# Performance work log

Measured on AMD Instinct MI355X. Metric: run time of the kernel, lower is better.

The kernel has to match this reference:

```python
import jax, jax.numpy as jnp
import numpy as np

D = 2048        # hidden_size
F = 1024        # moe_intermediate_size
E = 16          # num_experts
TOP_K = 2       # num_experts_per_tok
NORM_TOPK = True
B, S = 2, 1024


def setup_inputs() -> dict:
    key = jax.random.key(0)
    ks = jax.random.split(key, 6)
    scale = 0.02
    x = jax.random.normal(ks[0], (B, S, D), jnp.float32)
    w_gate = jax.random.normal(ks[1], (D, E), jnp.float32) * scale          # gate Linear (no bias)
    w_g = jax.random.normal(ks[2], (E, D, F), jnp.float32) * scale          # SwitchGLU gate_proj
    w_u = jax.random.normal(ks[3], (E, D, F), jnp.float32) * scale          # SwitchGLU up_proj
    w_d = jax.random.normal(ks[4], (E, F, D), jnp.float32) * scale          # SwitchGLU down_proj
    expert_bias = jnp.zeros((E,), jnp.float32)                              # nn.Parameter(zeros)
    return {"x": x, "w_gate": w_gate, "w_g": w_g, "w_u": w_u, "w_d": w_d,
            "expert_bias": expert_bias}


def reference(x, w_gate, w_g, w_u, w_d, expert_bias):
    xf = x.reshape(-1, D)  # [T, D] flatten tokens
    T = xf.shape[0]
    # routing: softmax in fp32, bias added AFTER softmax (as in source)
    gates = jax.nn.softmax((xf @ w_gate).astype(jnp.float32), axis=-1) + expert_bias
    scores, inds = jax.lax.top_k(gates, TOP_K)  # values gathered from biased gates
    if NORM_TOPK:
        scores = scores / (jnp.sum(scores, axis=-1, keepdims=True) + 1e-20)
    scores = scores.astype(x.dtype)
    # scatter top-k weights into dense [T, E] combine matrix (top-k inds are distinct)
    cw = jnp.zeros((T, E), x.dtype).at[jnp.arange(T)[:, None], inds].add(scores)
    # scan over experts: each step one gated-SiLU MLP + weighted accumulate
    def step(acc, inp):
        wg, wu, wd, w = inp  # wg/wu [D,F], wd [F,D], w [T]
        h = jax.nn.silu(xf @ wg) * (xf @ wu)  # [T, F]
        return acc + w[:, None] * (h @ wd), None
    y, _ = jax.lax.scan(step, jnp.zeros_like(xf), (w_g, w_u, w_d, cw.T))
    return y.reshape(x.shape)
```

## Files before the change

### kernel.cpp

```cpp
#include <hip/hip_runtime.h>
#include <hip/hip_bf16.h>

#define D_DIM 2048
#define F_DIM 1024
#define E_NUM 16
#define T_TOK 2048

typedef float f32x4 __attribute__((ext_vector_type(4)));
typedef short short8 __attribute__((ext_vector_type(8)));

__device__ inline unsigned pk2bf(float a, float b) {
    __hip_bfloat162 h2 = __float22bfloat162_rn(make_float2(a, b));
    union { __hip_bfloat162 h; unsigned u; } c; c.h = h2; return c.u;
}

__global__ __launch_bounds__(64) void k_route(const float* __restrict__ x,
                                              const float* __restrict__ wg,
                                              const float* __restrict__ bias,
                                              int* __restrict__ topk_idx,
                                              float* __restrict__ topk_w,
                                              int* __restrict__ counts) {
    int t = blockIdx.x;
    int l = threadIdx.x;
    int e = l & 15, c = l >> 4;
    const float* xr = x + (size_t)t * D_DIM + c * (D_DIM / 4);
    const float* wr = wg + (size_t)(c * (D_DIM / 4)) * E_NUM + e;
    float acc = 0.f;
#pragma unroll 4
    for (int d = 0; d < D_DIM / 4; ++d) acc += xr[d] * wr[(size_t)d * E_NUM];
    acc += __shfl_xor(acc, 16);
    acc += __shfl_xor(acc, 32);
    float m = acc;
#pragma unroll
    for (int s = 1; s < 16; s <<= 1) m = fmaxf(m, __shfl_xor(m, s));
    float p = __expf(acc - m);
    float sum = p;
#pragma unroll
    for (int s = 1; s < 16; s <<= 1) sum += __shfl_xor(sum, s);
    p = p / sum + bias[e];
    float v1 = p; int i1 = e;
#pragma unroll
    for (int s = 1; s < 16; s <<= 1) {
        float ov = __shfl_xor(v1, s); int oi = __shfl_xor(i1, s);
        if (ov > v1 || (ov == v1 && oi < i1)) { v1 = ov; i1 = oi; }
    }
    float v2 = (e == i1) ? -1e30f : p; int i2 = e;
#pragma unroll
    for (int s = 1; s < 16; s <<= 1) {
        float ov = __shfl_xor(v2, s); int oi = __shfl_xor(i2, s);
        if (ov > v2 || (ov == v2 && oi < i2)) { v2 = ov; i2 = oi; }
    }
    if (l == 0) {
        float s2 = v1 + v2 + 1e-20f;
        topk_idx[2 * t] = i1; topk_idx[2 * t + 1] = i2;
        topk_w[2 * t] = v1 / s2; topk_w[2 * t + 1] = v2 / s2;
        atomicAdd(&counts[i1], 1);
        atomicAdd(&counts[i2], 1);
    }
}

__global__ void k_offsets(const int* __restrict__ counts, int* __restrict__ offsets,
                          int* __restrict__ cursors) {
    if (threadIdx.x == 0) {
        int run = 0;
        for (int e = 0; e < E_NUM; ++e) { offsets[e] = run; cursors[e] = run; run += counts[e]; }
        offsets[E_NUM] = run;
    }
}

__global__ void k_scatter(const int* __restrict__ topk_idx, const float* __restrict__ topk_w,
                          int* __restrict__ cursors, int* __restrict__ token_ids,
                          float* __restrict__ slot_w) {
    int i = blockIdx.x * blockDim.x + threadIdx.x;
    if (i >= T_TOK * 2) return;
    int e = topk_idx[i];
    int slot = atomicAdd(&cursors[e], 1);
    token_ids[slot] = i >> 1;
    slot_w[slot] = topk_w[i];
}

__global__ __launch_bounds__(256, 3) void k_gateup(const float* __restrict__ x,
                                                   const float* __restrict__ wg_all,
                                                   const float* __restrict__ wu_all,
                                                   const int* __restrict__ offsets,
                                                   const int* __restrict__ token_ids,
                                                   __hip_bfloat16* __restrict__ hbuf) {
    int e = blockIdx.z;
    int off = offsets[e];
    int n_e = offsets[e + 1] - off;
    int m0 = blockIdx.y * 128;
    if (m0 >= n_e) return;
    int n0 = blockIdx.x * 64;
    const float* wg = wg_all + (size_t)e * (D_DIM * F_DIM);
    const float* wu = wu_all + (size_t)e * (D_DIM * F_DIM);

    __shared__ unsigned short As[2][128 * 40];
    __shared__ unsigned short Bs[2][2][64 * 40];

    int tid = threadIdx.x;
    int wid = tid >> 6, lane = tid & 63;
    int q = lane >> 4, nl = lane & 15;
    int wr = wid >> 1, wc = wid & 1;

    int arow = tid >> 1, acg = (tid & 1) * 16;
    int ag = m0 + arow;
    bool avalid = ag < n_e;
    const float* xrow = x + (size_t)(avalid ? token_ids[off + ag] : 0) * D_DIM;
    int bkr = (tid >> 4) * 2;
    int bcol = (tid & 15) * 4;

    f32x4 ra[4], rg[2], ru[2];
    f32x4 accG[4][2], accU[4][2];
#pragma unroll
    for (int ms = 0; ms < 4; ++ms)
#pragma unroll
        for (int ns = 0; ns < 2; ++ns) {
            accG[ms][ns] = (f32x4){0.f, 0.f, 0.f, 0.f};
            accU[ms][ns] = (f32x4){0.f, 0.f, 0.f, 0.f};
        }

    auto loadG = [&](int k0) {
#pragma unroll
        for (int j = 0; j < 4; ++j)
            ra[j] = avalid ? *(const f32x4*)(xrow + k0 + acg + 4 * j) : (f32x4){0.f, 0.f, 0.f, 0.f};
        size_t o0 = (size_t)(k0 + bkr) * F_DIM + n0 + bcol;
        rg[0] = *(const f32x4*)(wg + o0);
        rg[1] = *(const f32x4*)(wg + o0 + F_DIM);
        ru[0] = *(const f32x4*)(wu + o0);
        ru[1] = *(const f32x4*)(wu + o0 + F_DIM);
    };
    auto writeL = [&](int b) {
        unsigned short* a = &As[b][arow * 40 + acg];
        union { short8 v; unsigned u[4]; } w0, w1;
        w0.u[0] = pk2bf(ra[0].x, ra[0].y); w0.u[1] = pk2bf(ra[0].z, ra[0].w);
        w0.u[2] = pk2bf(ra[1].x, ra[1].y); w0.u[3] = pk2bf(ra[1].z, ra[1].w);
        w1.u[0] = pk2bf(ra[2].x, ra[2].y); w1.u[1] = pk2bf(ra[2].z, ra[2].w);
        w1.u[2] = pk2bf(ra[3].x, ra[3].y); w1.u[3] = pk2bf(ra[3].z, ra[3].w);
        *(short8*)a = w0.v; *(short8*)(a + 8) = w1.v;
#pragma unroll
        for (int j = 0; j < 4; ++j) {
            int col = bcol + j;
            int kk = bkr ^ (((col >> 3) & 3) << 3);
            *(unsigned*)&Bs[b][0][col * 40 + kk] = pk2bf(rg[0][j], rg[1][j]);
            *(unsigned*)&Bs[b][1][col * 40 + kk] = pk2bf(ru[0][j], ru[1][j]);
        }
    };
    auto compute = [&](int b) {
        short8 af[4];
#pragma unroll
        for (int ms = 0; ms < 4; ++ms)
            af[ms] = *(const short8*)&As[b][(wr * 64 + ms * 16 + nl) * 40 + q * 8];
#pragma unroll
        for (int ns = 0; ns < 2; ++ns) {
            int col = wc * 32 + ns * 16 + nl;
            int colb = col * 40 + 8 * (q ^ ((col >> 3) & 3));
            short8 bg = *(const short8*)&Bs[b][0][colb];
            short8 bu = *(const short8*)&Bs[b][1][colb];
#pragma unroll
            for (int ms = 0; ms < 4; ++ms) {
                accG[ms][ns] = __builtin_amdgcn_mfma_f32_16x16x32_bf16(af[ms], bg, accG[ms][ns], 0, 0, 0);
                accU[ms][ns] = __builtin_amdgcn_mfma_f32_16x16x32_bf16(af[ms], bu, accU[ms][ns], 0, 0, 0);
            }
        }
    };

    loadG(0);
    writeL(0);
    __syncthreads();
    for (int t = 0; t < D_DIM / 32; ++t) {
        int b = t & 1;
        if (t < D_DIM / 32 - 1) loadG((t + 1) * 32);
        compute(b);
        if (t < D_DIM / 32 - 1) writeL(b ^ 1);
        __syncthreads();
    }

#pragma unroll
    for (int ms = 0; ms < 4; ++ms)
#pragma unroll
        for (int j = 0; j < 4; ++j) {
            int g2 = m0 + wr * 64 + ms * 16 + q * 4 + j;
            if (g2 < n_e) {
                size_t hbase = (size_t)(off + g2) * F_DIM;
#pragma unroll
                for (int ns = 0; ns < 2; ++ns) {
                    float g = accG[ms][ns][j];
                    float u = accU[ms][ns][j];
                    float hv = (g / (1.f + __expf(-g))) * u;
                    hbuf[hbase + n0 + wc * 32 + ns * 16 + nl] = __float2bfloat16(hv);
                }
            }
        }
}

__global__ __launch_bounds__(256, 3) void k_down(const __hip_bfloat16* __restrict__ hbuf,
                                                 const float* __restrict__ wd_all,
                                                 const int* __restrict__ offsets,
                                                 const int* __restrict__ token_ids,
                                                 const float* __restrict__ slot_w,
                                                 float* __restrict__ y) {
    int e = blockIdx.z;
    int off = offsets[e];
    int n_e = offsets[e + 1] - off;
    int m0 = blockIdx.y * 128;
    if (m0 >= n_e) return;
    int n0 = blockIdx.x * 64;
    const float* wd = wd_all + (size_t)e * (F_DIM * D_DIM);

    __shared__ unsigned short As[2][128 * 40];
    __shared__ unsigned short Bs[2][64 * 40];

    int tid = threadIdx.x;
    int wid = tid >> 6, lane = tid & 63;
    int q = lane >> 4, nl = lane & 15;
    int wr = wid >> 1, wc = wid & 1;

    int arow = tid >> 1, acg = (tid & 1) * 16;
    int ag = m0 + arow;
    bool avalid = ag < n_e;
    const unsigned short* hrow = (const unsigned short*)hbuf + (size_t)(off + (avalid ? ag : 0)) * F_DIM;
    int bkr = (tid >> 4) * 2;
    int bcol = (tid & 15) * 4;

    short8 rh[2];
    f32x4 rd[2];
    f32x4 acc[4][2];
#pragma unroll
    for (int ms = 0; ms < 4; ++ms)
#pragma unroll
        for (int ns = 0; ns < 2; ++ns) acc[ms][ns] = (f32x4){0.f, 0.f, 0.f, 0.f};

    auto loadG = [&](int k0) {
        if (avalid) {
            rh[0] = *(const short8*)(hrow + k0 + acg);
            rh[1] = *(const short8*)(hrow + k0 + acg + 8);
        } else {
            rh[0] = (short8){0, 0, 0, 0, 0, 0, 0, 0};
            rh[1] = (short8){0, 0, 0, 0, 0, 0, 0, 0};
        }
        size_t o0 = (size_t)(k0 + bkr) * D_DIM + n0 + bcol;
        rd[0] = *(const f32x4*)(wd + o0);
        rd[1] = *(const f32x4*)(wd + o0 + D_DIM);
    };
    auto writeL = [&](int b) {
        unsigned short* a = &As[b][arow * 40 + acg];
        *(short8*)a = rh[0]; *(short8*)(a + 8) = rh[1];
#pragma unroll
        for (int j = 0; j < 4; ++j) {
            int col = bcol + j;
            int kk = bkr ^ (((col >> 3) & 3) << 3);
            *(unsigned*)&Bs[b][col * 40 + kk] = pk2bf(rd[0][j], rd[1][j]);
        }
    };
    auto compute = [&](int b) {
        short8 af[4];
#pragma unroll
        for (int ms = 0; ms < 4; ++ms)
            af[ms] = *(const short8*)&As[b][(wr * 64 + ms * 16 + nl) * 40 + q * 8];
#pragma unroll
        for (int ns = 0; ns < 2; ++ns) {
            int col = wc * 32 + ns * 16 + nl;
            short8 bd = *(const short8*)&Bs[b][col * 40 + 8 * (q ^ ((col >> 3) & 3))];
#pragma unroll
            for (int ms = 0; ms < 4; ++ms)
                acc[ms][ns] = __builtin_amdgcn_mfma_f32_16x16x32_bf16(af[ms], bd, acc[ms][ns], 0, 0, 0);
        }
    };

    loadG(0);
    writeL(0);
    __syncthreads();
    for (int t = 0; t < F_DIM / 32; ++t) {
        int b = t & 1;
        if (t < F_DIM / 32 - 1) loadG((t + 1) * 32);
        compute(b);
        if (t < F_DIM / 32 - 1) writeL(b ^ 1);
        __syncthreads();
    }

#pragma unroll
    for (int ms = 0; ms < 4; ++ms)
#pragma unroll
        for (int j = 0; j < 4; ++j) {
            int g2 = m0 + wr * 64 + ms * 16 + q * 4 + j;
            if (g2 < n_e) {
                float w2 = slot_w[off + g2];
                int t = token_ids[off + g2];
#pragma unroll
                for (int ns = 0; ns < 2; ++ns)
                    atomicAdd(&y[(size_t)t * D_DIM + n0 + wc * 32 + ns * 16 + nl], acc[ms][ns][j] * w2);
            }
        }
}

extern "C" void kernel_launch(void* const* d_in, const int* in_sizes, int n_in,
                              void* d_out, int out_size, void* d_ws, size_t ws_size,
                              hipStream_t stream) {
    const float* x      = (const float*)d_in[0];
    const float* w_gate = (const float*)d_in[1];
    const float* w_g    = (const float*)d_in[2];
    const float* w_u    = (const float*)d_in[3];
    const float* w_d    = (const float*)d_in[4];
    const float* bias   = (const float*)d_in[5];
    float* y = (float*)d_out;

    char* ws = (char*)d_ws;
    int*   counts    = (int*)(ws + 0);
    int*   offsets   = (int*)(ws + 64);
    int*   cursors   = (int*)(ws + 192);
    int*   topk_idx  = (int*)(ws + 256);
    float* topk_w    = (float*)(ws + 256 + 16384);
    int*   token_ids = (int*)(ws + 256 + 32768);
    float* slot_w    = (float*)(ws + 256 + 49152);
    __hip_bfloat16* hbuf = (__hip_bfloat16*)(ws + 66048);

    hipMemsetAsync(ws, 0, 256, stream);
    hipMemsetAsync(d_out, 0, (size_t)out_size * sizeof(float), stream);

    k_route<<<T_TOK, 64, 0, stream>>>(x, w_gate, bias, topk_idx, topk_w, counts);
    k_offsets<<<1, 64, 0, stream>>>(counts, offsets, cursors);
    k_scatter<<<(T_TOK * 2 + 255) / 256, 256, 0, stream>>>(topk_idx, topk_w, cursors, token_ids, slot_w);
    k_gateup<<<dim3(F_DIM / 64, 16, E_NUM), 256, 0, stream>>>(x, w_g, w_u, offsets, token_ids, hbuf);
    k_down<<<dim3(D_DIM / 64, 16, E_NUM), 256, 0, stream>>>(hbuf, w_d, offsets, token_ids, slot_w, y);
}
```

Measured before the change: 329.8 us.

## Deepen global prefetch to two stages with explicit waitcnt and sched barriers

```diff
diff --git a/kernel.cpp b/kernel.cpp
--- a/kernel.cpp
+++ b/kernel.cpp
@@ -8,6 +8,13 @@
 
 typedef float f32x4 __attribute__((ext_vector_type(4)));
 typedef short short8 __attribute__((ext_vector_type(8)));
+
+#define VM8 asm volatile("s_waitcnt vmcnt(8)" ::: "memory")
+#define VM4 asm volatile("s_waitcnt vmcnt(4)" ::: "memory")
+#define VM0 asm volatile("s_waitcnt vmcnt(0)" ::: "memory")
+#define LGKM0 asm volatile("s_waitcnt lgkmcnt(0)" ::: "memory")
+#define SB0 __builtin_amdgcn_sched_barrier(0)
+#define SBAR __builtin_amdgcn_s_barrier()
 
 __device__ inline unsigned pk2bf(float a, float b) {
     __hip_bfloat162 h2 = __float22bfloat162_rn(make_float2(a, b));
@@ -79,7 +86,7 @@
     slot_w[slot] = topk_w[i];
 }
 
-__global__ __launch_bounds__(256, 3) void k_gateup(const float* __restrict__ x,
+__global__ __launch_bounds__(256, 2) void k_gateup(const float* __restrict__ x,
                                                    const float* __restrict__ wg_all,
                                                    const float* __restrict__ wu_all,
                                                    const int* __restrict__ offsets,
@@ -105,11 +112,12 @@
     int arow = tid >> 1, acg = (tid & 1) * 16;
     int ag = m0 + arow;
     bool avalid = ag < n_e;
-    const float* xrow = x + (size_t)(avalid ? token_ids[off + ag] : 0) * D_DIM;
+    const float* xrow = x + (size_t)token_ids[off + (avalid ? ag : 0)] * D_DIM;
     int bkr = (tid >> 4) * 2;
     int bcol = (tid & 15) * 4;
 
-    f32x4 ra[4], rg[2], ru[2];
+    f32x4 raA[4], rgA[2], ruA[2];
+    f32x4 raB[4], rgB[2], ruB[2];
     f32x4 accG[4][2], accU[4][2];
 #pragma unroll
     for (int ms = 0; ms < 4; ++ms)
@@ -119,30 +127,54 @@
             accU[ms][ns] = (f32x4){0.f, 0.f, 0.f, 0.f};
         }
 
-    auto loadG = [&](int k0) {
-#pragma unroll
-        for (int j = 0; j < 4; ++j)
-            ra[j] = avalid ? *(const f32x4*)(xrow + k0 + acg + 4 * j) : (f32x4){0.f, 0.f, 0.f, 0.f};
+    auto loadGA = [&](int k0) {
+#pragma unroll
+        for (int j = 0; j < 4; ++j) raA[j] = *(const f32x4*)(xrow + k0 + acg + 4 * j);
         size_t o0 = (size_t)(k0 + bkr) * F_DIM + n0 + bcol;
-        rg[0] = *(const f32x4*)(wg + o0);
-        rg[1] = *(const f32x4*)(wg + o0 + F_DIM);
-        ru[0] = *(const f32x4*)(wu + o0);
-        ru[1] = *(const f32x4*)(wu + o0 + F_DIM);
-    };
-    auto writeL = [&](int b) {
-        unsigned short* a = &As[b][arow * 40 + acg];
+        rgA[0] = *(const f32x4*)(wg + o0);
+        rgA[1] = *(const f32x4*)(wg + o0 + F_DIM);
+        ruA[0] = *(const f32x4*)(wu + o0);
+        ruA[1] = *(const f32x4*)(wu + o0 + F_DIM);
+    };
+    auto loadGB = [&](int k0) {
+#pragma unroll
+        for (int j = 0; j < 4; ++j) raB[j] = *(const f32x4*)(xrow + k0 + acg + 4 * j);
+        size_t o0 = (size_t)(k0 + bkr) * F_DIM + n0 + bcol;
+        rgB[0] = *(const f32x4*)(wg + o0);
+        rgB[1] = *(const f32x4*)(wg + o0 + F_DIM);
+        ruB[0] = *(const f32x4*)(wu + o0);
+        ruB[1] = *(const f32x4*)(wu + o0 + F_DIM);
+    };
+    auto writeLA = [&]() {
+        unsigned short* a = &As[0][arow * 40 + acg];
         union { short8 v; unsigned u[4]; } w0, w1;
-        w0.u[0] = pk2bf(ra[0].x, ra[0].y); w0.u[1] = pk2bf(ra[0].z, ra[0].w);
-        w0.u[2] = pk2bf(ra[1].x, ra[1].y); w0.u[3] = pk2bf(ra[1].z, ra[1].w);
-        w1.u[0] = pk2bf(ra[2].x, ra[2].y); w1.u[1] = pk2bf(ra[2].z, ra[2].w);
-        w1.u[2] = pk2bf(ra[3].x, ra[3].y); w1.u[3] = pk2bf(ra[3].z, ra[3].w);
+        w0.u[0] = pk2bf(raA[0].x, raA[0].y); w0.u[1] = pk2bf(raA[0].z, raA[0].w);
+        w0.u[2] = pk2bf(raA[1].x, raA[1].y); w0.u[3] = pk2bf(raA[1].z, raA[1].w);
+        w1.u[0] = pk2bf(raA[2].x, raA[2].y); w1.u[1] = pk2bf(raA[2].z, raA[2].w);
+        w1.u[2] = pk2bf(raA[3].x, raA[3].y); w1.u[3] = pk2bf(raA[3].z, raA[3].w);
         *(short8*)a = w0.v; *(short8*)(a + 8) = w1.v;
 #pragma unroll
         for (int j = 0; j < 4; ++j) {
             int col = bcol + j;
             int kk = bkr ^ (((col >> 3) & 3) << 3);
-            *(unsigned*)&Bs[b][0][col * 40 + kk] = pk2bf(rg[0][j], rg[1][j]);
-            *(unsigned*)&Bs[b][1][col * 40 + kk] = pk2bf(ru[0][j], ru[1][j]);
+            *(unsigned*)&Bs[0][0][col * 40 + kk] = pk2bf(rgA[0][j], rgA[1][j]);
+            *(unsigned*)&Bs[0][1][col * 40 + kk] = pk2bf(ruA[0][j], ruA[1][j]);
+        }
+    };
+    auto writeLB = [&]() {
+        unsigned short* a = &As[1][arow * 40 + acg];
+        union { short8 v; unsigned u[4]; } w0, w1;
+        w0.u[0] = pk2bf(raB[0].x, raB[0].y); w0.u[1] = pk2bf(raB[0].z, raB[0].w);
+        w0.u[2] = pk2bf(raB[1].x, raB[1].y); w0.u[3] = pk2bf(raB[1].z, raB[1].w);
+        w1.u[0] = pk2bf(raB[2].x, raB[2].y); w1.u[1] = pk2bf(raB[2].z, raB[2].w);
+        w1.u[2] = pk2bf(raB[3].x, raB[3].y); w1.u[3] = pk2bf(raB[3].z, raB[3].w);
+        *(short8*)a = w0.v; *(short8*)(a + 8) = w1.v;
+#pragma unroll
+        for (int j = 0; j < 4; ++j) {
+            int col = bcol + j;
+            int kk = bkr ^ (((col >> 3) & 3) << 3);
+            *(unsigned*)&Bs[1][0][col * 40 + kk] = pk2bf(rgB[0][j], rgB[1][j]);
+            *(unsigned*)&Bs[1][1][col * 40 + kk] = pk2bf(ruB[0][j], ruB[1][j]);
         }
     };
     auto compute = [&](int b) {
@@ -164,15 +196,27 @@
         }
     };
 
-    loadG(0);
-    writeL(0);
-    __syncthreads();
-    for (int t = 0; t < D_DIM / 32; ++t) {
-        int b = t & 1;
-        if (t < D_DIM / 32 - 1) loadG((t + 1) * 32);
-        compute(b);
-        if (t < D_DIM / 32 - 1) writeL(b ^ 1);
-        __syncthreads();
+    const int NT = D_DIM / 32;
+    loadGA(0);
+    loadGB(32);
+    VM8; SB0;
+    writeLA();
+    LGKM0; SB0; SBAR; SB0;
+    for (int t = 0; t < NT; t += 2) {
+        if (t + 2 < NT) loadGA((t + 2) * 32);
+        compute(0);
+        if (t + 2 < NT) { VM8; } else { VM0; }
+        SB0;
+        writeLB();
+        LGKM0; SB0; SBAR; SB0;
+        if (t + 3 < NT) loadGB((t + 3) * 32);
+        compute(1);
+        if (t + 2 < NT) {
+            if (t + 4 < NT) { VM8; } else { VM0; }
+            SB0;
+            writeLA();
+            LGKM0; SB0; SBAR; SB0;
+        }
     }
 
 #pragma unroll
@@ -193,7 +237,7 @@
         }
 }
 
-__global__ __launch_bounds__(256, 3) void k_down(const __hip_bfloat16* __restrict__ hbuf,
+__global__ __launch_bounds__(256, 2) void k_down(const __hip_bfloat16* __restrict__ hbuf,
                                                  const float* __restrict__ wd_all,
                                                  const int* __restrict__ offsets,
                                                  const int* __restrict__ token_ids,
@@ -222,34 +266,46 @@
     int bkr = (tid >> 4) * 2;
     int bcol = (tid & 15) * 4;
 
-    short8 rh[2];
-    f32x4 rd[2];
+    short8 rhA[2], rhB[2];
+    f32x4 rdA[2], rdB[2];
     f32x4 acc[4][2];
 #pragma unroll
     for (int ms = 0; ms < 4; ++ms)
 #pragma unroll
         for (int ns = 0; ns < 2; ++ns) acc[ms][ns] = (f32x4){0.f, 0.f, 0.f, 0.f};
 
-    auto loadG = [&](int k0) {
-        if (avalid) {
-            rh[0] = *(const short8*)(hrow + k0 + acg);
-            rh[1] = *(const short8*)(hrow + k0 + acg + 8);
-        } else {
-            rh[0] = (short8){0, 0, 0, 0, 0, 0, 0, 0};
-            rh[1] = (short8){0, 0, 0, 0, 0, 0, 0, 0};
-        }
+    auto loadGA = [&](int k0) {
+        rhA[0] = *(const short8*)(hrow + k0 + acg);
+        rhA[1] = *(const short8*)(hrow + k0 + acg + 8);
         size_t o0 = (size_t)(k0 + bkr) * D_DIM + n0 + bcol;
-        rd[0] = *(const f32x4*)(wd + o0);
-        rd[1] = *(const f32x4*)(wd + o0 + D_DIM);
-    };
-    auto writeL = [&](int b) {
-        unsigned short* a = &As[b][arow * 40 + acg];
-        *(short8*)a = rh[0]; *(short8*)(a + 8) = rh[1];
+        rdA[0] = *(const f32x4*)(wd + o0);
+        rdA[1] = *(const f32x4*)(wd + o0 + D_DIM);
+    };
+    auto loadGB = [&](int k0) {
+        rhB[0] = *(const short8*)(hrow + k0 + acg);
+        rhB[1] = *(const short8*)(hrow + k0 + acg + 8);
+        size_t o0 = (size_t)(k0 + bkr) * D_DIM + n0 + bcol;
+        rdB[0] = *(const f32x4*)(wd + o0);
+        rdB[1] = *(const f32x4*)(wd + o0 + D_DIM);
+    };
+    auto writeLA = [&]() {
+        unsigned short* a = &As[0][arow * 40 + acg];
+        *(short8*)a = rhA[0]; *(short8*)(a + 8) = rhA[1];
 #pragma unroll
         for (int j = 0; j < 4; ++j) {
             int col = bcol + j;
             int kk = bkr ^ (((col >> 3) & 3) << 3);
-            *(unsigned*)&Bs[b][col * 40 + kk] = pk2bf(rd[0][j], rd[1][j]);
+            *(unsigned*)&Bs[0][col * 40 + kk] = pk2bf(rdA[0][j], rdA[1][j]);
+        }
+    };
+    auto writeLB = [&]() {
+        unsigned short* a = &As[1][arow * 40 + acg];
+        *(short8*)a = rhB[0]; *(short8*)(a + 8) = rhB[1];
+#pragma unroll
+        for (int j = 0; j < 4; ++j) {
+            int col = bcol + j;
+            int kk = bkr ^ (((col >> 3) & 3) << 3);
+            *(unsigned*)&Bs[1][col * 40 + kk] = pk2bf(rdB[0][j], rdB[1][j]);
         }
     };
     auto compute = [&](int b) {
@@ -267,15 +323,27 @@
         }
     };
 
-    loadG(0);
-    writeL(0);
-    __syncthreads();
-    for (int t = 0; t < F_DIM / 32; ++t) {
-        int b = t & 1;
-        if (t < F_DIM / 32 - 1) loadG((t + 1) * 32);
-        compute(b);
-        if (t < F_DIM / 32 - 1) writeL(b ^ 1);
-        __syncthreads();
+    const int NT = F_DIM / 32;
+    loadGA(0);
+    loadGB(32);
+    VM4; SB0;
+    writeLA();
+    LGKM0; SB0; SBAR; SB0;
+    for (int t = 0; t < NT; t += 2) {
+        if (t + 2 < NT) loadGA((t + 2) * 32);
+        compute(0);
+        if (t + 2 < NT) { VM4; } else { VM0; }
+        SB0;
+        writeLB();
+        LGKM0; SB0; SBAR; SB0;
+        if (t + 3 < NT) loadGB((t + 3) * 32);
+        compute(1);
+        if (t + 2 < NT) {
+            if (t + 4 < NT) { VM4; } else { VM0; }
+            SB0;
+            writeLA();
+            LGKM0; SB0; SBAR; SB0;
+        }
     }
 
 #pragma unroll
```

Measured after the change: 360.0 us. +9.2%, slower.

## Pre-gather tokens to bf16 and widen GEMM tiles to 128x128 with 512 threads

Applied to the files above, without the earlier changes.

```diff
diff --git a/kernel.cpp b/kernel.cpp
--- a/kernel.cpp
+++ b/kernel.cpp
@@ -5,9 +5,11 @@
 #define F_DIM 1024
 #define E_NUM 16
 #define T_TOK 2048
+#define NSLOT (T_TOK * 2)
 
 typedef float f32x4 __attribute__((ext_vector_type(4)));
 typedef short short8 __attribute__((ext_vector_type(8)));
+typedef unsigned uint2v __attribute__((ext_vector_type(2)));
 
 __device__ inline unsigned pk2bf(float a, float b) {
     __hip_bfloat162 h2 = __float22bfloat162_rn(make_float2(a, b));
@@ -72,44 +74,60 @@
                           int* __restrict__ cursors, int* __restrict__ token_ids,
                           float* __restrict__ slot_w) {
     int i = blockIdx.x * blockDim.x + threadIdx.x;
-    if (i >= T_TOK * 2) return;
+    if (i >= NSLOT) return;
     int e = topk_idx[i];
     int slot = atomicAdd(&cursors[e], 1);
     token_ids[slot] = i >> 1;
     slot_w[slot] = topk_w[i];
 }
 
-__global__ __launch_bounds__(256, 3) void k_gateup(const float* __restrict__ x,
+__global__ __launch_bounds__(256) void k_gather(const float* __restrict__ x,
+                                                const int* __restrict__ token_ids,
+                                                __hip_bfloat16* __restrict__ xg) {
+    int s = blockIdx.x;
+    const float* src = x + (size_t)token_ids[s] * D_DIM + threadIdx.x * 8;
+    f32x4 a = *(const f32x4*)src;
+    f32x4 b = *(const f32x4*)(src + 4);
+    union { short8 v; unsigned u[4]; } w;
+    w.u[0] = pk2bf(a.x, a.y); w.u[1] = pk2bf(a.z, a.w);
+    w.u[2] = pk2bf(b.x, b.y); w.u[3] = pk2bf(b.z, b.w);
+    *(short8*)((unsigned short*)xg + (size_t)s * D_DIM + threadIdx.x * 8) = w.v;
+}
+
+__global__ __launch_bounds__(512, 2) void k_gateup(const __hip_bfloat16* __restrict__ xg,
                                                    const float* __restrict__ wg_all,
                                                    const float* __restrict__ wu_all,
                                                    const int* __restrict__ offsets,
-                                                   const int* __restrict__ token_ids,
                                                    __hip_bfloat16* __restrict__ hbuf) {
     int e = blockIdx.z;
     int off = offsets[e];
     int n_e = offsets[e + 1] - off;
     int m0 = blockIdx.y * 128;
     if (m0 >= n_e) return;
-    int n0 = blockIdx.x * 64;
+    int n0 = blockIdx.x * 128;
     const float* wg = wg_all + (size_t)e * (D_DIM * F_DIM);
     const float* wu = wu_all + (size_t)e * (D_DIM * F_DIM);
 
     __shared__ unsigned short As[2][128 * 40];
-    __shared__ unsigned short Bs[2][2][64 * 40];
+    __shared__ unsigned short Bs[2][2][128 * 40];
 
     int tid = threadIdx.x;
     int wid = tid >> 6, lane = tid & 63;
     int q = lane >> 4, nl = lane & 15;
-    int wr = wid >> 1, wc = wid & 1;
-
-    int arow = tid >> 1, acg = (tid & 1) * 16;
-    int ag = m0 + arow;
-    bool avalid = ag < n_e;
-    const float* xrow = x + (size_t)(avalid ? token_ids[off + ag] : 0) * D_DIM;
-    int bkr = (tid >> 4) * 2;
-    int bcol = (tid & 15) * 4;
-
-    f32x4 ra[4], rg[2], ru[2];
+    int wm = wid >> 2, wn = wid & 3;
+
+    int arow = tid >> 2, acg = (tid & 3) * 8;
+    int sg = off + m0 + arow; if (sg > NSLOT - 1) sg = NSLOT - 1;
+    const unsigned short* xrow = (const unsigned short*)xg + (size_t)sg * D_DIM;
+
+    int bmat = tid >> 8;
+    int t8 = tid & 255;
+    int bcol = (t8 & 31) * 4;
+    int bk4 = (t8 >> 5) * 4;
+    const float* wmat = bmat ? wu : wg;
+
+    short8 rA;
+    f32x4 rw[4];
     f32x4 accG[4][2], accU[4][2];
 #pragma unroll
     for (int ms = 0; ms < 4; ++ms)
@@ -120,39 +138,31 @@
         }
 
     auto loadG = [&](int k0) {
-#pragma unroll
-        for (int j = 0; j < 4; ++j)
-            ra[j] = avalid ? *(const f32x4*)(xrow + k0 + acg + 4 * j) : (f32x4){0.f, 0.f, 0.f, 0.f};
-        size_t o0 = (size_t)(k0 + bkr) * F_DIM + n0 + bcol;
-        rg[0] = *(const f32x4*)(wg + o0);
-        rg[1] = *(const f32x4*)(wg + o0 + F_DIM);
-        ru[0] = *(const f32x4*)(wu + o0);
-        ru[1] = *(const f32x4*)(wu + o0 + F_DIM);
+        rA = *(const short8*)(xrow + k0 + acg);
+        const float* p = wmat + (size_t)(k0 + bk4) * F_DIM + n0 + bcol;
+#pragma unroll
+        for (int i = 0; i < 4; ++i) rw[i] = *(const f32x4*)(p + (size_t)i * F_DIM);
     };
     auto writeL = [&](int b) {
-        unsigned short* a = &As[b][arow * 40 + acg];
-        union { short8 v; unsigned u[4]; } w0, w1;
-        w0.u[0] = pk2bf(ra[0].x, ra[0].y); w0.u[1] = pk2bf(ra[0].z, ra[0].w);
-        w0.u[2] = pk2bf(ra[1].x, ra[1].y); w0.u[3] = pk2bf(ra[1].z, ra[1].w);
-        w1.u[0] = pk2bf(ra[2].x, ra[2].y); w1.u[1] = pk2bf(ra[2].z, ra[2].w);
-        w1.u[2] = pk2bf(ra[3].x, ra[3].y); w1.u[3] = pk2bf(ra[3].z, ra[3].w);
-        *(short8*)a = w0.v; *(short8*)(a + 8) = w1.v;
+        *(short8*)&As[b][arow * 40 + acg] = rA;
 #pragma unroll
         for (int j = 0; j < 4; ++j) {
             int col = bcol + j;
-            int kk = bkr ^ (((col >> 3) & 3) << 3);
-            *(unsigned*)&Bs[b][0][col * 40 + kk] = pk2bf(rg[0][j], rg[1][j]);
-            *(unsigned*)&Bs[b][1][col * 40 + kk] = pk2bf(ru[0][j], ru[1][j]);
+            int kk = bk4 ^ (((col >> 3) & 3) << 3);
+            uint2v v;
+            v[0] = pk2bf(rw[0][j], rw[1][j]);
+            v[1] = pk2bf(rw[2][j], rw[3][j]);
+            *(uint2v*)&Bs[b][bmat][col * 40 + kk] = v;
         }
     };
     auto compute = [&](int b) {
         short8 af[4];
 #pragma unroll
         for (int ms = 0; ms < 4; ++ms)
-            af[ms] = *(const short8*)&As[b][(wr * 64 + ms * 16 + nl) * 40 + q * 8];
+            af[ms] = *(const short8*)&As[b][(wm * 64 + ms * 16 + nl) * 40 + q * 8];
 #pragma unroll
         for (int ns = 0; ns < 2; ++ns) {
-            int col = wc * 32 + ns * 16 + nl;
+            int col = wn * 32 + ns * 16 + nl;
             int colb = col * 40 + 8 * (q ^ ((col >> 3) & 3));
             short8 bg = *(const short8*)&Bs[b][0][colb];
             short8 bu = *(const short8*)&Bs[b][1][colb];
@@ -179,21 +189,21 @@
     for (int ms = 0; ms < 4; ++ms)
 #pragma unroll
         for (int j = 0; j < 4; ++j) {
-            int g2 = m0 + wr * 64 + ms * 16 + q * 4 + j;
-            if (g2 < n_e) {
-                size_t hbase = (size_t)(off + g2) * F_DIM;
+            int r = m0 + wm * 64 + ms * 16 + q * 4 + j;
+            if (r < n_e) {
+                size_t hbase = (size_t)(off + r) * F_DIM;
 #pragma unroll
                 for (int ns = 0; ns < 2; ++ns) {
                     float g = accG[ms][ns][j];
                     float u = accU[ms][ns][j];
                     float hv = (g / (1.f + __expf(-g))) * u;
-                    hbuf[hbase + n0 + wc * 32 + ns * 16 + nl] = __float2bfloat16(hv);
+                    hbuf[hbase + n0 + wn * 32 + ns * 16 + nl] = __float2bfloat16(hv);
                 }
             }
         }
 }
 
-__global__ __launch_bounds__(256, 3) void k_down(const __hip_bfloat16* __restrict__ hbuf,
+__global__ __launch_bounds__(512, 4) void k_down(const __hip_bfloat16* __restrict__ hbuf,
                                                  const float* __restrict__ wd_all,
                                                  const int* __restrict__ offsets,
                                                  const int* __restrict__ token_ids,
@@ -204,25 +214,25 @@
     int n_e = offsets[e + 1] - off;
     int m0 = blockIdx.y * 128;
     if (m0 >= n_e) return;
-    int n0 = blockIdx.x * 64;
+    int n0 = blockIdx.x * 128;
     const float* wd = wd_all + (size_t)e * (F_DIM * D_DIM);
 
     __shared__ unsigned short As[2][128 * 40];
-    __shared__ unsigned short Bs[2][64 * 40];
+    __shared__ unsigned short Bs[2][128 * 40];
 
     int tid = threadIdx.x;
     int wid = tid >> 6, lane = tid & 63;
     int q = lane >> 4, nl = lane & 15;
-    int wr = wid >> 1, wc = wid & 1;
-
-    int arow = tid >> 1, acg = (tid & 1) * 16;
-    int ag = m0 + arow;
-    bool avalid = ag < n_e;
-    const unsigned short* hrow = (const unsigned short*)hbuf + (size_t)(off + (avalid ? ag : 0)) * F_DIM;
-    int bkr = (tid >> 4) * 2;
-    int bcol = (tid & 15) * 4;
-
-    short8 rh[2];
+    int wm = wid >> 2, wn = wid & 3;
+
+    int arow = tid >> 2, acg = (tid & 3) * 8;
+    int sg = off + m0 + arow; if (sg > NSLOT - 1) sg = NSLOT - 1;
+    const unsigned short* hrow = (const unsigned short*)hbuf + (size_t)sg * F_DIM;
+
+    int bcol = (tid & 31) * 4;
+    int bk2 = (tid >> 5) * 2;
+
+    short8 rA;
     f32x4 rd[2];
     f32x4 acc[4][2];
 #pragma unroll
@@ -231,24 +241,17 @@
         for (int ns = 0; ns < 2; ++ns) acc[ms][ns] = (f32x4){0.f, 0.f, 0.f, 0.f};
 
     auto loadG = [&](int k0) {
-        if (avalid) {
-            rh[0] = *(const short8*)(hrow + k0 + acg);
-            rh[1] = *(const short8*)(hrow + k0 + acg + 8);
-        } else {
-            rh[0] = (short8){0, 0, 0, 0, 0, 0, 0, 0};
-            rh[1] = (short8){0, 0, 0, 0, 0, 0, 0, 0};
-        }
-        size_t o0 = (size_t)(k0 + bkr) * D_DIM + n0 + bcol;
+        rA = *(const short8*)(hrow + k0 + acg);
+        size_t o0 = (size_t)(k0 + bk2) * D_DIM + n0 + bcol;
         rd[0] = *(const f32x4*)(wd + o0);
         rd[1] = *(const f32x4*)(wd + o0 + D_DIM);
     };
     auto writeL = [&](int b) {
-        unsigned short* a = &As[b][arow * 40 + acg];
-        *(short8*)a = rh[0]; *(short8*)(a + 8) = rh[1];
+        *(short8*)&As[b][arow * 40 + acg] = rA;
 #pragma unroll
         for (int j = 0; j < 4; ++j) {
             int col = bcol + j;
-            int kk = bkr ^ (((col >> 3) & 3) << 3);
+            int kk = bk2 ^ (((col >> 3) & 3) << 3);
             *(unsigned*)&Bs[b][col * 40 + kk] = pk2bf(rd[0][j], rd[1][j]);
         }
     };
@@ -256,10 +259,10 @@
         short8 af[4];
 #pragma unroll
         for (int ms = 0; ms < 4; ++ms)
-            af[ms] = *(const short8*)&As[b][(wr * 64 + ms * 16 + nl) * 40 + q * 8];
+            af[ms] = *(const short8*)&As[b][(wm * 64 + ms * 16 + nl) * 40 + q * 8];
 #pragma unroll
         for (int ns = 0; ns < 2; ++ns) {
-            int col = wc * 32 + ns * 16 + nl;
+            int col = wn * 32 + ns * 16 + nl;
             short8 bd = *(const short8*)&Bs[b][col * 40 + 8 * (q ^ ((col >> 3) & 3))];
 #pragma unroll
             for (int ms = 0; ms < 4; ++ms)
@@ -282,13 +285,13 @@
     for (int ms = 0; ms < 4; ++ms)
 #pragma unroll
         for (int j = 0; j < 4; ++j) {
-            int g2 = m0 + wr * 64 + ms * 16 + q * 4 + j;
-            if (g2 < n_e) {
-                float w2 = slot_w[off + g2];
-                int t = token_ids[off + g2];
+            int r = m0 + wm * 64 + ms * 16 + q * 4 + j;
+            if (r < n_e) {
+                float w2 = slot_w[off + r];
+                int t = token_ids[off + r];
 #pragma unroll
                 for (int ns = 0; ns < 2; ++ns)
-                    atomicAdd(&y[(size_t)t * D_DIM + n0 + wc * 32 + ns * 16 + nl], acc[ms][ns][j] * w2);
+                    atomicAdd(&y[(size_t)t * D_DIM + n0 + wn * 32 + ns * 16 + nl], acc[ms][ns][j] * w2);
             }
         }
 }
@@ -313,13 +316,15 @@
     int*   token_ids = (int*)(ws + 256 + 32768);
     float* slot_w    = (float*)(ws + 256 + 49152);
     __hip_bfloat16* hbuf = (__hip_bfloat16*)(ws + 66048);
+    __hip_bfloat16* xg   = (__hip_bfloat16*)(ws + 66048 + 8388608);
 
     hipMemsetAsync(ws, 0, 256, stream);
     hipMemsetAsync(d_out, 0, (size_t)out_size * sizeof(float), stream);
 
     k_route<<<T_TOK, 64, 0, stream>>>(x, w_gate, bias, topk_idx, topk_w, counts);
     k_offsets<<<1, 64, 0, stream>>>(counts, offsets, cursors);
-    k_scatter<<<(T_TOK * 2 + 255) / 256, 256, 0, stream>>>(topk_idx, topk_w, cursors, token_ids, slot_w);
-    k_gateup<<<dim3(F_DIM / 64, 16, E_NUM), 256, 0, stream>>>(x, w_g, w_u, offsets, token_ids, hbuf);
-    k_down<<<dim3(D_DIM / 64, 16, E_NUM), 256, 0, stream>>>(hbuf, w_d, offsets, token_ids, slot_w, y);
-}
+    k_scatter<<<(NSLOT + 255) / 256, 256, 0, stream>>>(topk_idx, topk_w, cursors, token_ids, slot_w);
+    k_gather<<<NSLOT, 256, 0, stream>>>(x, token_ids, xg);
+    k_gateup<<<dim3(F_DIM / 128, 16, E_NUM), 512, 0, stream>>>(xg, w_g, w_u, offsets, hbuf);
+    k_down<<<dim3(D_DIM / 128, 16, E_NUM), 512, 0, stream>>>(hbuf, w_d, offsets, token_ids, slot_w, y);
+}
```

After: 421.9 us. 1.28x slower.
